# Performance work log

Measured on AMD Instinct MI355X. Metric: run time of the kernel, lower is better.

The kernel has to match this reference:

```python
import jax, jax.numpy as jnp
import numpy as np

HEADS = 8
DIM_HEAD = 64


def setup_inputs() -> dict:
    key = jax.random.key(0)
    ks = jax.random.split(key, 6)
    B, Nq, Nk, Dq = 4, 2048, 2048, 1024
    inner = HEADS * DIM_HEAD  # 512
    return {
        "x": jax.random.normal(ks[0], (B, Nq, Dq), jnp.float32),
        "context": jax.random.normal(ks[1], (B, Nk, Dq), jnp.float32),
        "Wq": jax.random.normal(ks[2], (Dq, inner), jnp.float32) * 0.02,
        "Wkv": jax.random.normal(ks[3], (Dq, 2 * inner), jnp.float32) * 0.02,
        "Wout": jax.random.normal(ks[4], (inner, Dq), jnp.float32) * 0.02,
        "bout": jax.random.normal(ks[5], (Dq,), jnp.float32) * 0.02,
        "topk": 64,
    }


def reference(x, context, Wq, Wkv, Wout, bout, topk):
    B, Nq, _ = x.shape
    Nk = context.shape[1]
    H, D = HEADS, DIM_HEAD
    scale = D ** -0.5

    # projections: b n (h d) -> b h n d
    q = (x @ Wq).reshape(B, Nq, H, D).transpose(0, 2, 1, 3)
    kv = context @ Wkv
    k, v = jnp.split(kv, 2, axis=-1)
    k = k.reshape(B, Nk, H, D).transpose(0, 2, 1, 3)
    v = v.reshape(B, Nk, H, D).transpose(0, 2, 1, 3)

    sim = jnp.einsum('bhid,bhjd->bhij', q, k) * scale  # [B,H,Nq,Nk]

    # top-k sparsification: keep only topk keys per query, mask rest to -max
    k_eff = min(int(topk), Nk)
    _, idx = jax.lax.top_k(sim, k_eff)  # [B,H,Nq,k_eff]
    keep = jnp.zeros(sim.shape, dtype=bool)
    bi = jnp.arange(B)[:, None, None, None]
    hi = jnp.arange(H)[None, :, None, None]
    qi = jnp.arange(Nq)[None, None, :, None]
    keep = keep.at[bi, hi, qi, idx].set(True)
    max_neg = -jnp.finfo(sim.dtype).max
    sim = jnp.where(keep, sim, max_neg)

    attn = jax.nn.softmax(sim, axis=-1)
    out = jnp.einsum('bhij,bhjd->bhid', attn, v)
    out = out.transpose(0, 2, 1, 3).reshape(B, Nq, H * D)
    return out @ Wout + bout
```

## Files before the change

kernel.cpp:

```cpp
#include <hip/hip_runtime.h>
#include <math.h>

#define BATCH 4
#define NQ 2048
#define NK 2048
#define DQ 1024
#define NHEADS 8
#define DHEAD 64
#define INNER (NHEADS*DHEAD)
#define NROWS (BATCH*NHEADS*NQ)
#define CAND_MAX 128

using frag_ab = __attribute__((ext_vector_type(8))) short;
using frag_cd = __attribute__((ext_vector_type(4))) float;
using u16x8   = __attribute__((ext_vector_type(8))) unsigned short;

static __device__ __forceinline__ unsigned short f32_to_bf16_rne(float f) {
  unsigned u = __float_as_uint(f);
  u += 0x7FFFu + ((u >> 16) & 1u);
  return (unsigned short)(u >> 16);
}

static __device__ __forceinline__ void split_trunc(float f, unsigned short& h, unsigned short& l) {
  unsigned u = __float_as_uint(f);
  h = (unsigned short)(u >> 16);
  float hf = __uint_as_float(u & 0xFFFF0000u);
  unsigned r = __float_as_uint(f - hf);
  l = (unsigned short)(r >> 16);
}

static __device__ __forceinline__ void split3(float f, unsigned short& h,
                                              unsigned short& m, unsigned short& l) {
  unsigned u = __float_as_uint(f);
  h = (unsigned short)(u >> 16);
  float hf = __uint_as_float(u & 0xFFFF0000u);
  float r1 = f - hf;
  unsigned u1 = __float_as_uint(r1);
  m = (unsigned short)(u1 >> 16);
  float mf = __uint_as_float(u1 & 0xFFFF0000u);
  float r2 = r1 - mf;
  l = (unsigned short)(__float_as_uint(r2) >> 16);
}

__global__ __launch_bounds__(256) void split_wT3(
    const float* __restrict__ W, int ldw, int coloff, int K, int N,
    unsigned short* __restrict__ TH, unsigned short* __restrict__ TM,
    unsigned short* __restrict__ TL)
{
  __shared__ float tile[32*33];
  const int k0 = blockIdx.x * 32, n0 = blockIdx.y * 32;
  const int t = threadIdx.x;
  {
    int lk = t >> 3, ln4 = (t & 7) * 4;
    const float4 v = *(const float4*)(W + (size_t)(k0 + lk)*ldw + coloff + n0 + ln4);
    tile[lk*33 + ln4+0] = v.x;
    tile[lk*33 + ln4+1] = v.y;
    tile[lk*33 + ln4+2] = v.z;
    tile[lk*33 + ln4+3] = v.w;
  }
  __syncthreads();
  int n = t >> 3, k4 = (t & 7) * 4;
  #pragma unroll
  for (int j = 0; j < 4; ++j) {
    unsigned short h, m, l;
    split3(tile[(k4+j)*33 + n], h, m, l);
    size_t o = (size_t)(n0 + n)*K + k0 + k4 + j;
    TH[o] = h; TM[o] = m; TL[o] = l;
  }
}

__global__ __launch_bounds__(256) void split_wT(
    const float* __restrict__ W, int ldw, int coloff, int K, int N,
    unsigned short* __restrict__ TH, unsigned short* __restrict__ TL)
{
  __shared__ float tile[32*33];
  const int k0 = blockIdx.x * 32, n0 = blockIdx.y * 32;
  const int t = threadIdx.x;
  {
    int lk = t >> 3, ln4 = (t & 7) * 4;
    const float4 v = *(const float4*)(W + (size_t)(k0 + lk)*ldw + coloff + n0 + ln4);
    tile[lk*33 + ln4+0] = v.x;
    tile[lk*33 + ln4+1] = v.y;
    tile[lk*33 + ln4+2] = v.z;
    tile[lk*33 + ln4+3] = v.w;
  }
  __syncthreads();
  int n = t >> 3, k4 = (t & 7) * 4;
  #pragma unroll
  for (int j = 0; j < 4; ++j) {
    unsigned short h, l;
    split_trunc(tile[(k4+j)*33 + n], h, l);
    TH[(size_t)(n0 + n)*K + k0 + k4 + j] = h;
    TL[(size_t)(n0 + n)*K + k0 + k4 + j] = l;
  }
}

__global__ __launch_bounds__(512) void gemm_mfma6_proj(
    const float* __restrict__ A,
    const unsigned short* __restrict__ BtH, const unsigned short* __restrict__ BtM,
    const unsigned short* __restrict__ BtL,
    float* __restrict__ C32,
    unsigned short* __restrict__ Hi, unsigned short* __restrict__ Lo)
{
  extern __shared__ unsigned short smp[];
  unsigned short* ah = smp;
  unsigned short* am = ah + 128*40;
  unsigned short* al = am + 128*40;
  unsigned short* bh = al + 128*40;
  unsigned short* bm = bh + 64*40;
  unsigned short* bl = bm + 64*40;

  const int t = threadIdx.x;
  const int w = t >> 6, l = t & 63;
  const int lr = l & 15, quad = l >> 4;
  const int bid = (int)blockIdx.x;
  const int lid = (bid & 7) * 64 + (bid >> 3);
  const int n0 = (lid & 7) * 64, m0 = (lid >> 3) * 128;

  frag_cd acc[4];
  #pragma unroll
  for (int nt = 0; nt < 4; ++nt)
    acc[nt] = (frag_cd){0.f, 0.f, 0.f, 0.f};

  for (int kt = 0; kt < DQ; kt += 32) {
    {
      int row = t >> 2, k8 = (t & 3) * 8;
      const float* src = A + (size_t)(m0 + row) * DQ + kt + k8;
      float4 v0 = *(const float4*)(src);
      float4 v1 = *(const float4*)(src + 4);
      float vv[8] = {v0.x, v0.y, v0.z, v0.w, v1.x, v1.y, v1.z, v1.w};
      unsigned short h8[8], m8[8], l8[8];
      #pragma unroll
      for (int j = 0; j < 8; ++j) split3(vv[j], h8[j], m8[j], l8[j]);
      *(u16x8*)(ah + row*40 + k8) = *(u16x8*)h8;
      *(u16x8*)(am + row*40 + k8) = *(u16x8*)m8;
      *(u16x8*)(al + row*40 + k8) = *(u16x8*)l8;
    }
    if (t < 256) {
      int n = t >> 2, k8 = (t & 3) * 8;
      size_t o = (size_t)(n0 + n)*DQ + kt + k8;
      *(u16x8*)(bh + n*40 + k8) = *(const u16x8*)(BtH + o);
      *(u16x8*)(bm + n*40 + k8) = *(const u16x8*)(BtM + o);
      *(u16x8*)(bl + n*40 + k8) = *(const u16x8*)(BtL + o);
    }
    __syncthreads();
    {
      int row = w*16 + lr;
      frag_ab aH = *(const frag_ab*)(ah + row*40 + quad*8);
      frag_ab aM = *(const frag_ab*)(am + row*40 + quad*8);
      frag_ab aL = *(const frag_ab*)(al + row*40 + quad*8);
      #pragma unroll
      for (int nt = 0; nt < 4; ++nt) {
        int bn = nt*16 + lr;
        frag_ab bH_ = *(const frag_ab*)(bh + bn*40 + quad*8);
        frag_ab bM_ = *(const frag_ab*)(bm + bn*40 + quad*8);
        frag_ab bL_ = *(const frag_ab*)(bl + bn*40 + quad*8);
        frag_cd c = acc[nt];
        c = __builtin_amdgcn_mfma_f32_16x16x32_bf16(aL, bH_, c, 0, 0, 0);
        c = __builtin_amdgcn_mfma_f32_16x16x32_bf16(aH, bL_, c, 0, 0, 0);
        c = __builtin_amdgcn_mfma_f32_16x16x32_bf16(aM, bM_, c, 0, 0, 0);
        c = __builtin_amdgcn_mfma_f32_16x16x32_bf16(aM, bH_, c, 0, 0, 0);
        c = __builtin_amdgcn_mfma_f32_16x16x32_bf16(aH, bM_, c, 0, 0, 0);
        c = __builtin_amdgcn_mfma_f32_16x16x32_bf16(aH, bH_, c, 0, 0, 0);
        acc[nt] = c;
      }
    }
    __syncthreads();
  }

  #pragma unroll
  for (int nt = 0; nt < 4; ++nt) {
    int cc = n0 + nt*16 + lr;
    int h = cc >> 6, d = cc & 63;
    #pragma unroll
    for (int i = 0; i < 4; ++i) {
      int r = m0 + w*16 + quad*4 + i;
      int b = r >> 11, n = r & (NQ - 1);
      size_t idx = (((size_t)(b*NHEADS + h))*NQ + n)*64 + d;
      float vf = acc[nt][i];
      C32[idx] = vf;
      unsigned short hb = f32_to_bf16_rne(vf);
      float hf = __uint_as_float((unsigned)hb << 16);
      unsigned short lb = f32_to_bf16_rne(vf - hf);
      Hi[idx] = hb;
      Lo[idx] = lb;
    }
  }
}

template<int MODE>
__global__ __launch_bounds__(256) void gemm_mfma3(
    const float* __restrict__ A, int lda,
    const unsigned short* __restrict__ BtH, const unsigned short* __restrict__ BtL,
    int K, int N, const float* __restrict__ bias, float* __restrict__ C0)
{
  __shared__ unsigned short ah[128*72];
  __shared__ unsigned short al[128*72];
  __shared__ unsigned short bh2[64*72];
  __shared__ unsigned short bl2[64*72];
  const int t = threadIdx.x;
  const int w = t >> 6, l = t & 63;
  const int lr = l & 15, quad = l >> 4;
  const int n0 = blockIdx.x * 64, m0 = blockIdx.y * 128;

  frag_cd acc[2][4];
  #pragma unroll
  for (int ms = 0; ms < 2; ++ms)
    #pragma unroll
    for (int nt = 0; nt < 4; ++nt)
      acc[ms][nt] = (frag_cd){0.f, 0.f, 0.f, 0.f};

  for (int kt = 0; kt < K; kt += 64) {
    #pragma unroll
    for (int i = 0; i < 4; ++i) {
      int idx = i*256 + t;
      int row = idx >> 3, k8 = (idx & 7) * 8;
      const float* src = A + (size_t)(m0 + row) * lda + kt + k8;
      float4 v0 = *(const float4*)(src);
      float4 v1 = *(const float4*)(src + 4);
      float vv[8] = {v0.x, v0.y, v0.z, v0.w, v1.x, v1.y, v1.z, v1.w};
      unsigned short h8[8], l8[8];
      #pragma unroll
      for (int j = 0; j < 8; ++j) split_trunc(vv[j], h8[j], l8[j]);
      *(u16x8*)(ah + row*72 + k8) = *(u16x8*)h8;
      *(u16x8*)(al + row*72 + k8) = *(u16x8*)l8;
    }
    #pragma unroll
    for (int i = 0; i < 2; ++i) {
      int idx = i*256 + t;
      int n = idx >> 3, k8 = (idx & 7) * 8;
      *(u16x8*)(bh2 + n*72 + k8) = *(const u16x8*)(BtH + (size_t)(n0 + n)*K + kt + k8);
      *(u16x8*)(bl2 + n*72 + k8) = *(const u16x8*)(BtL + (size_t)(n0 + n)*K + kt + k8);
    }
    __syncthreads();
    #pragma unroll
    for (int ks = 0; ks < 2; ++ks) {
      frag_ab aH[2], aL[2], bH[4], bL[4];
      #pragma unroll
      for (int ms = 0; ms < 2; ++ms) {
        int row = w*32 + ms*16 + lr;
        aH[ms] = *(const frag_ab*)(ah + row*72 + ks*32 + quad*8);
        aL[ms] = *(const frag_ab*)(al + row*72 + ks*32 + quad*8);
      }
      #pragma unroll
      for (int nt = 0; nt < 4; ++nt) {
        int row = nt*16 + lr;
        bH[nt] = *(const frag_ab*)(bh2 + row*72 + ks*32 + quad*8);
        bL[nt] = *(const frag_ab*)(bl2 + row*72 + ks*32 + quad*8);
      }
      #pragma unroll
      for (int ms = 0; ms < 2; ++ms)
        #pragma unroll
        for (int nt = 0; nt < 4; ++nt) {
          acc[ms][nt] = __builtin_amdgcn_mfma_f32_16x16x32_bf16(aH[ms], bH[nt], acc[ms][nt], 0, 0, 0);
          acc[ms][nt] = __builtin_amdgcn_mfma_f32_16x16x32_bf16(aH[ms], bL[nt], acc[ms][nt], 0, 0, 0);
          acc[ms][nt] = __builtin_amdgcn_mfma_f32_16x16x32_bf16(aL[ms], bH[nt], acc[ms][nt], 0, 0, 0);
        }
    }
    __syncthreads();
  }

  #pragma unroll
  for (int ms = 0; ms < 2; ++ms)
    #pragma unroll
    for (int nt = 0; nt < 4; ++nt) {
      int cc = n0 + nt*16 + lr;
      #pragma unroll
      for (int i = 0; i < 4; ++i) {
        int r = m0 + w*32 + ms*16 + quad*4 + i;
        float v = acc[ms][nt][i];
        if (MODE == 0) {
          C0[(size_t)r * N + cc] = v + bias[cc];
        } else {
          int b = r >> 11, n = r & (NQ - 1);
          int h = cc >> 6, d = cc & 63;
          C0[(((size_t)(b*NHEADS + h))*NK + n)*64 + d] = v;
        }
      }
    }
}

__global__ __launch_bounds__(256) void score_mfma(
    const unsigned short* __restrict__ Qhi, const unsigned short* __restrict__ Qlo,
    const unsigned short* __restrict__ Khi, const unsigned short* __restrict__ Klo,
    unsigned short* __restrict__ S16, int bh0)
{
  extern __shared__ unsigned short sm[];
  unsigned short* qh = sm;
  unsigned short* ql = qh + 128*72;
  unsigned short* kh = ql + 128*72;
  unsigned short* kl = kh + 128*72;

  const int t  = threadIdx.x;
  const int qt = blockIdx.x, kt = blockIdx.y;
  const int bh = bh0 + blockIdx.z;
  const size_t qbase = ((size_t)bh*NQ + qt*128) * 64;
  const size_t kbase = ((size_t)bh*NK + kt*128) * 64;

  #pragma unroll
  for (int i = 0; i < 4; ++i) {
    int c   = t + i*256;
    int row = c >> 3, off = (c & 7) * 8;
    *(u16x8*)(qh + row*72 + off) = *(const u16x8*)(Qhi + qbase + row*64 + off);
    *(u16x8*)(ql + row*72 + off) = *(const u16x8*)(Qlo + qbase + row*64 + off);
    *(u16x8*)(kh + row*72 + off) = *(const u16x8*)(Khi + kbase + row*64 + off);
    *(u16x8*)(kl + row*72 + off) = *(const u16x8*)(Klo + kbase + row*64 + off);
  }
  __syncthreads();

  const int w = t >> 6, l = t & 63;
  const int quad = l >> 4, lr = l & 15;

  frag_ab aH[2][2], aL[2][2];
  #pragma unroll
  for (int qs = 0; qs < 2; ++qs) {
    int row = w*32 + qs*16 + lr;
    #pragma unroll
    for (int s = 0; s < 2; ++s) {
      aH[qs][s] = *(const frag_ab*)(qh + row*72 + s*32 + quad*8);
      aL[qs][s] = *(const frag_ab*)(ql + row*72 + s*32 + quad*8);
    }
  }

  for (int ks = 0; ks < 8; ++ks) {
    frag_ab bH[2], bL[2];
    int krow = ks*16 + lr;
    #pragma unroll
    for (int s = 0; s < 2; ++s) {
      bH[s] = *(const frag_ab*)(kh + krow*72 + s*32 + quad*8);
      bL[s] = *(const frag_ab*)(kl + krow*72 + s*32 + quad*8);
    }
    #pragma unroll
    for (int qs = 0; qs < 2; ++qs) {
      frag_cd c = {0.f, 0.f, 0.f, 0.f};
      #pragma unroll
      for (int s = 0; s < 2; ++s) {
        c = __builtin_amdgcn_mfma_f32_16x16x32_bf16(aH[qs][s], bH[s], c, 0, 0, 0);
        c = __builtin_amdgcn_mfma_f32_16x16x32_bf16(aH[qs][s], bL[s], c, 0, 0, 0);
        c = __builtin_amdgcn_mfma_f32_16x16x32_bf16(aL[qs][s], bH[s], c, 0, 0, 0);
      }
      int qrow = qt*128 + w*32 + qs*16 + quad*4;
      int kcol = kt*128 + ks*16 + lr;
      size_t base = ((size_t)blockIdx.z * NQ + qrow) * NK + kcol;
      #pragma unroll
      for (int i = 0; i < 4; ++i) {
        _Float16 h = (_Float16)(c[i] * 0.125f);
        S16[base + (size_t)i*NK] = __builtin_bit_cast(unsigned short, h);
      }
    }
  }
}

__global__ __launch_bounds__(256) void select_rows(
    const unsigned short* __restrict__ S16, unsigned short* __restrict__ cand,
    int* __restrict__ cnt, const int* __restrict__ topkp, int row0)
{
  const int t = threadIdx.x;
  const int w = t >> 6, l = t & 63;
  const int rl = blockIdx.x * 4 + w;
  const size_t row = (size_t)row0 + rl;
  const unsigned short* Sr = S16 + (size_t)rl * NK;
  const unsigned long long lmask = (1ull << l) - 1ull;

  int kEff = *topkp;
  if (kEff > CAND_MAX) kEff = CAND_MAX;
  if (kEff < 1) kEff = 1;

  unsigned uv[32];
  #pragma unroll
  for (int c = 0; c < 32; ++c) {
    unsigned bb = Sr[c*64 + l];
    uv[c] = (bb & 0x8000u) ? (~bb & 0xFFFFu) : (bb | 0x8000u);
  }
  unsigned lo_ = 0u, hi_ = 0xFFFFu;
  while (lo_ < hi_) {
    unsigned mid = (lo_ + hi_ + 1u) >> 1;
    int c_ = 0;
    #pragma unroll
    for (int c = 0; c < 32; ++c) c_ += (uv[c] >= mid) ? 1 : 0;
    #pragma unroll
    for (int off = 32; off > 0; off >>= 1) c_ += __shfl_xor(c_, off);
    if (c_ >= kEff) lo_ = mid; else hi_ = mid - 1;
  }
  unsigned short sb = (lo_ & 0x8000u) ? (unsigned short)(lo_ & 0x7FFFu)
                                      : (unsigned short)(~lo_ & 0xFFFFu);
  float skth = (float)__builtin_bit_cast(_Float16, sb);
  float smarg = skth - 3e-3f;
  _Float16 hm = (_Float16)smarg;
  unsigned short mb = __builtin_bit_cast(unsigned short, hm);
  unsigned um = (mb & 0x8000u) ? (~(unsigned)mb & 0xFFFFu) : ((unsigned)mb | 0x8000u);

  int base = 0;
  for (int c = 0; c < 32; ++c) {
    bool pred = (uv[c] >= um);
    unsigned long long msk = __ballot(pred);
    if (pred) {
      int pos = base + __popcll(msk & lmask);
      if (pos < CAND_MAX) cand[row*CAND_MAX + pos] = (unsigned short)(c*64 + l);
    }
    base += __popcll(msk);
  }
  if (l == 0) cnt[row] = (base < CAND_MAX) ? base : CAND_MAX;
}

__global__ __launch_bounds__(256) void attn_phase_b(
    const float* __restrict__ Q32, const float* __restrict__ K32,
    const float* __restrict__ V32, const unsigned short* __restrict__ cand,
    const int* __restrict__ cnt, float* __restrict__ inner,
    const int* __restrict__ topkp)
{
  __shared__ uint2 pvbuf[4][128];

  const int t = threadIdx.x;
  const int w = t >> 6, l = t & 63;
  const int nwg = (int)gridDim.x;
  const int bid = (int)blockIdx.x;
  const int swz = (bid & 7) * (nwg >> 3) + (bid >> 3);
  const size_t row = (size_t)swz * 4 + w;
  const int bh = (int)(row >> 11);
  const int q  = (int)(row & (NQ - 1));
  const unsigned long long lmask = (1ull << l) - 1ull;

  int kEff = *topkp;
  if (kEff > CAND_MAX) kEff = CAND_MAX;
  if (kEff < 1) kEff = 1;
  int m = cnt[row];
  if (kEff > m) kEff = m;

  const float* Kb = K32 + (size_t)bh * NK * 64;
  const float* Vb = V32 + (size_t)bh * NK * 64;

  const int g = l >> 3, r = l & 7;
  double2 q2[4];
  #pragma unroll
  for (int i = 0; i < 4; ++i) {
    float2 qf = *(const float2*)(Q32 + row*64 + i*16 + r*2);
    q2[i].x = (double)qf.x;
    q2[i].y = (double)qf.y;
  }

  int ck[2];
  ck[0] = cand[row*CAND_MAX + l];
  ck[1] = cand[row*CAND_MAX + 64 + l];
  double cs[2] = {-INFINITY, -INFINITY};
  unsigned long long cu[2] = {0ull, 0ull};

  #define RESCORE_PASS(P, C)                                                  \
  {                                                                           \
    const int j = (P)*8 + g;                                                  \
    const bool valid = (j < m);                                               \
    int key = __shfl(ck[C], j & 63);                                          \
    const float* kp = Kb + (size_t)(valid ? key : 0) * 64;                    \
    double s0 = 0.0, s1 = 0.0;                                                \
    _Pragma("unroll")                                                         \
    for (int i = 0; i < 4; ++i) {                                             \
      float2 kv = *(const float2*)(kp + i*16 + r*2);                          \
      s0 = fma((double)kv.x, q2[i].x, s0);                                    \
      s1 = fma((double)kv.y, q2[i].y, s1);                                    \
    }                                                                         \
    double s = s0 + s1;                                                       \
    s += __shfl_xor(s, 1);                                                    \
    s += __shfl_xor(s, 2);                                                    \
    s += __shfl_xor(s, 4);                                                    \
    s *= 0.125;                                                               \
    double sc = __shfl(s, (l & 7) * 8);                                       \
    const int pp = (P) & 7;                                                   \
    if ((l >> 3) == pp && ((C)*64 + pp*8 + (l & 7)) < m) {                    \
      unsigned long long b = (unsigned long long)__double_as_longlong(sc);    \
      cs[C] = sc;                                                             \
      cu[C] = (b >> 63) ? ~b : (b | 0x8000000000000000ull);                   \
    }                                                                         \
  }

  if (m <= 64) {
    #pragma unroll
    for (int p = 0; p < 8; ++p) RESCORE_PASS(p, 0)
  } else {
    #pragma unroll
    for (int p = 0; p < 8; ++p) RESCORE_PASS(p, 0)
    const int np2 = 8 + ((m - 64 + 7) >> 3);
    for (int p = 8; p < np2; ++p) RESCORE_PASS(p, 1)
  }
  #undef RESCORE_PASS

  const unsigned hu0 = (unsigned)(cu[0] >> 32), lu0 = (unsigned)cu[0];
  const unsigned hu1 = (unsigned)(cu[1] >> 32), lu1 = (unsigned)cu[1];

  unsigned T32 = 0u;
  for (int bit = 31; bit >= 0; --bit) {
    unsigned cT = T32 | (1u << bit);
    int tot = __popcll(__ballot(hu0 >= cT)) + __popcll(__ballot(hu1 >= cT));
    if (tot >= kEff) T32 = cT;
  }
  unsigned Tlo;
  {
    int cgt32 = __popcll(__ballot(hu0 > T32)) + __popcll(__ballot(hu1 > T32));
    bool e0 = (hu0 == T32), e1 = (hu1 == T32);
    unsigned long long bm0 = __ballot(e0), bm1 = __ballot(e1);
    int ceq = __popcll(bm0) + __popcll(bm1);
    int nEq32 = kEff - cgt32;
    if (ceq == 1) {
      Tlo = bm0 ? __shfl(lu0, (int)__builtin_ctzll(bm0))
                : __shfl(lu1, (int)__builtin_ctzll(bm1));
    } else {
      unsigned TL = 0u;
      for (int bit = 31; bit >= 0; --bit) {
        unsigned cT = TL | (1u << bit);
        int tot = __popcll(__ballot(e0 && lu0 >= cT))
                + __popcll(__ballot(e1 && lu1 >= cT));
        if (tot >= nEq32) TL = cT;
      }
      Tlo = TL;
    }
  }
  const unsigned long long T = ((unsigned long long)T32 << 32) | Tlo;

  double s_kth;
  { unsigned long long bb = (T >> 63) ? (T & 0x7FFFFFFFFFFFFFFFull) : ~T;
    s_kth = __longlong_as_double((long long)bb); }

  double nx = -INFINITY;
  #pragma unroll
  for (int c = 0; c < 2; ++c) { double v = (cu[c] < T) ? cs[c] : -INFINITY; nx = fmax(nx, v); }
  #pragma unroll
  for (int off = 32; off > 0; off >>= 1) nx = fmax(nx, __shfl_xor(nx, off));

  double smax = fmax(cs[0], cs[1]);
  #pragma unroll
  for (int off = 32; off > 0; off >>= 1) smax = fmax(smax, __shfl_xor(smax, off));

  const double DELTA = 5e-6;
  float wgt[2];
  if (!(s_kth - nx < 2.0*DELTA)) {
    int cgt = __popcll(__ballot(cu[0] > T)) + __popcll(__ballot(cu[1] > T));
    int nEq = kEff - cgt;
    int eqBase = 0;
    #pragma unroll
    for (int c = 0; c < 2; ++c) {
      bool eq = (cu[c] == T);
      unsigned long long eqm = __ballot(eq);
      int er = __popcll(eqm & lmask);
      bool sel = (cu[c] > T) || (eq && (eqBase + er) < nEq);
      eqBase += __popcll(eqm);
      wgt[c] = sel ? expf((float)(cs[c] - smax)) : 0.f;
    }
  } else {
    double cmid = 0.5 * (s_kth + nx);
    #pragma unroll
    for (int c = 0; c < 2; ++c) {
      double mu = 0.5 + (cs[c] - cmid) / (2.0*DELTA);
      mu = fmin(1.0, fmax(0.0, mu));
      wgt[c] = (float)mu * expf((float)(cs[c] - smax));
    }
  }

  pvbuf[w][l]      = make_uint2((unsigned)ck[0] & (NK - 1), __float_as_uint(wgt[0]));
  pvbuf[w][64 + l] = make_uint2((unsigned)ck[1] & (NK - 1), __float_as_uint(wgt[1]));
  float wsum = wgt[0] + wgt[1];
  #pragma unroll
  for (int off = 32; off > 0; off >>= 1) wsum += __shfl_xor(wsum, off);
  asm volatile("s_waitcnt lgkmcnt(0)" ::: "memory");

  const int sub = l >> 4;
  const int dl  = l & 15;
  const float* Vb4 = Vb + dl * 4;
  float ax = 0.f, ay = 0.f, az = 0.f, aw = 0.f;
  const int mm4 = (m + 3) & ~3;
  #pragma unroll 4
  for (int j0 = 0; j0 < mm4; j0 += 4) {
    uint2 p = pvbuf[w][j0 + sub];
    float wj = __uint_as_float(p.y);
    const float4 v = *(const float4*)(Vb4 + ((size_t)p.x << 6));
    ax = fmaf(wj, v.x, ax);
    ay = fmaf(wj, v.y, ay);
    az = fmaf(wj, v.z, az);
    aw = fmaf(wj, v.w, aw);
  }
  #pragma unroll
  for (int off = 32; off >= 16; off >>= 1) {
    ax += __shfl_xor(ax, off);
    ay += __shfl_xor(ay, off);
    az += __shfl_xor(az, off);
    aw += __shfl_xor(aw, off);
  }
  if (sub == 0) {
    int b = bh >> 3, h = bh & 7;
    float inv = 1.0f / wsum;
    float4 o;
    o.x = ax * inv; o.y = ay * inv; o.z = az * inv; o.w = aw * inv;
    *(float4*)(inner + ((size_t)b*NQ + q)*INNER + h*DHEAD + dl*4) = o;
  }
}

extern "C" void kernel_launch(void* const* d_in, const int* in_sizes, int n_in,
                              void* d_out, int out_size, void* d_ws, size_t ws_size,
                              hipStream_t stream)
{
  const float* x    = (const float*)d_in[0];
  const float* ctx  = (const float*)d_in[1];
  const float* Wq   = (const float*)d_in[2];
  const float* Wkv  = (const float*)d_in[3];
  const float* Wout = (const float*)d_in[4];
  const float* bout = (const float*)d_in[5];
  const int*   topk = (const int*)d_in[6];
  float* out = (float*)d_out;

  const size_t SZ = (size_t)BATCH * NHEADS * NQ * DHEAD;

  size_t off = 0;
  char* base = (char*)d_ws;
  auto take = [&](size_t bytes) { char* r = base + off; off += (bytes + 255) & ~(size_t)255; return r; };
  float* Q32 = (float*)take(SZ * sizeof(float));
  float* K32 = (float*)take(SZ * sizeof(float));
  unsigned short* cand = (unsigned short*)take((size_t)NROWS * CAND_MAX * 2);
  int* cnt = (int*)take((size_t)NROWS * sizeof(int));
  unsigned short* Qhi = (unsigned short*)take(SZ * 2);
  unsigned short* Qlo = (unsigned short*)take(SZ * 2);
  unsigned short* Khi = (unsigned short*)take(SZ * 2);
  unsigned short* Klo = (unsigned short*)take(SZ * 2);
  char* slab = base + off;

  const size_t WSZ = (size_t)INNER * DQ * 2;
  unsigned short* WqTH = (unsigned short*)(slab + 0*WSZ);
  unsigned short* WqTM = (unsigned short*)(slab + 1*WSZ);
  unsigned short* WqTL = (unsigned short*)(slab + 2*WSZ);
  unsigned short* WkTH = (unsigned short*)(slab + 3*WSZ);
  unsigned short* WkTM = (unsigned short*)(slab + 4*WSZ);
  unsigned short* WkTL = (unsigned short*)(slab + 5*WSZ);
  unsigned short* S16 = (unsigned short*)slab;
  unsigned short* WvTH = (unsigned short*)(slab + 0*WSZ);
  unsigned short* WvTL = (unsigned short*)(slab + 1*WSZ);
  unsigned short* WoTH = (unsigned short*)(slab + 2*WSZ);
  unsigned short* WoTL = (unsigned short*)(slab + 3*WSZ);
  float* V32   = (float*)Qhi;
  float* inner = (float*)Khi;

  const size_t per_bh = (size_t)NQ * NK * sizeof(unsigned short);
  size_t avail = (ws_size > off) ? (ws_size - off) : 0;
  int bhchunk = (int)(avail / per_bh);
  if (bhchunk < 1)  bhchunk = 1;
  if (bhchunk > 32) bhchunk = 32;

  const int M = BATCH * NQ;
  const int SCORE_LDS = 4 * 128 * 72 * (int)sizeof(unsigned short);
  const int PROJ_LDS  = 6 * 64 * 40 * (int)sizeof(unsigned short) * 2;
  hipFuncSetAttribute(reinterpret_cast<const void*>(score_mfma),
                      hipFuncAttributeMaxDynamicSharedMemorySize, SCORE_LDS);
  hipFuncSetAttribute(reinterpret_cast<const void*>(gemm_mfma6_proj),
                      hipFuncAttributeMaxDynamicSharedMemorySize, PROJ_LDS);

  split_wT3<<<dim3(DQ/32, INNER/32), 256, 0, stream>>>(Wq,  INNER,   0, DQ, INNER, WqTH, WqTM, WqTL);
  split_wT3<<<dim3(DQ/32, INNER/32), 256, 0, stream>>>(Wkv, 2*INNER, 0, DQ, INNER, WkTH, WkTM, WkTL);

  gemm_mfma6_proj<<<dim3((INNER/64)*(M/128)), 512, PROJ_LDS, stream>>>(x,   WqTH, WqTM, WqTL, Q32, Qhi, Qlo);
  gemm_mfma6_proj<<<dim3((INNER/64)*(M/128)), 512, PROJ_LDS, stream>>>(ctx, WkTH, WkTM, WkTL, K32, Khi, Klo);

  for (int c0 = 0; c0 < BATCH*NHEADS; c0 += bhchunk) {
    int cc = BATCH*NHEADS - c0; if (cc > bhchunk) cc = bhchunk;
    score_mfma<<<dim3(NQ/128, NK/128, cc), 256, SCORE_LDS, stream>>>(
        Qhi, Qlo, Khi, Klo, S16, c0);
    select_rows<<<dim3(cc*NQ/4), 256, 0, stream>>>(S16, cand, cnt, topk, c0*NQ);
  }

  split_wT<<<dim3(DQ/32, INNER/32), 256, 0, stream>>>(Wkv, 2*INNER, INNER, DQ, INNER, WvTH, WvTL);
  split_wT<<<dim3(INNER/32, DQ/32), 256, 0, stream>>>(Wout, DQ, 0, INNER, DQ, WoTH, WoTL);

  gemm_mfma3<2><<<dim3(INNER/64, M/128), 256, 0, stream>>>(ctx, DQ, WvTH, WvTL, DQ, INNER, nullptr, V32);
  attn_phase_b<<<dim3(NROWS/4), 256, 0, stream>>>(Q32, K32, V32, cand, cnt, inner, topk);
  gemm_mfma3<0><<<dim3(DQ/64, M/128), 256, 0, stream>>>(inner, INNER, WoTH, WoTL, INNER, DQ, bout, out);
}
```

Measured before the change: 723.0 us.

## Store score tiles in permuted layout with 16-byte vector writes and reads

The QK score kernel now keeps all eight k-slice accumulators per row in registers and writes each row's values as one 16-byte vector instead of scattered 2-byte stores. This produces a permuted column layout within each 128-key tile. The select kernel reads its 32 values per lane as four 16-byte loads and maps each candidate position back to the true key index through a bit permutation. This trades more accumulator registers for coalesced wide memory traffic on the large fp16 score buffer.

```diff
diff --git a/kernel.cpp b/kernel.cpp
--- a/kernel.cpp
+++ b/kernel.cpp
@@ -322,6 +322,8 @@
     }
   }
 
+  frag_cd c[2][8];
+  #pragma unroll
   for (int ks = 0; ks < 8; ++ks) {
     frag_ab bH[2], bL[2];
     int krow = ks*16 + lr;
@@ -332,23 +334,31 @@
     }
     #pragma unroll
     for (int qs = 0; qs < 2; ++qs) {
-      frag_cd c = {0.f, 0.f, 0.f, 0.f};
+      frag_cd cc = {0.f, 0.f, 0.f, 0.f};
       #pragma unroll
       for (int s = 0; s < 2; ++s) {
-        c = __builtin_amdgcn_mfma_f32_16x16x32_bf16(aH[qs][s], bH[s], c, 0, 0, 0);
-        c = __builtin_amdgcn_mfma_f32_16x16x32_bf16(aH[qs][s], bL[s], c, 0, 0, 0);
-        c = __builtin_amdgcn_mfma_f32_16x16x32_bf16(aL[qs][s], bH[s], c, 0, 0, 0);
-      }
-      int qrow = qt*128 + w*32 + qs*16 + quad*4;
-      int kcol = kt*128 + ks*16 + lr;
-      size_t base = ((size_t)blockIdx.z * NQ + qrow) * NK + kcol;
-      #pragma unroll
-      for (int i = 0; i < 4; ++i) {
-        _Float16 h = (_Float16)(c[i] * 0.125f);
-        S16[base + (size_t)i*NK] = __builtin_bit_cast(unsigned short, h);
-      }
-    }
-  }
+        cc = __builtin_amdgcn_mfma_f32_16x16x32_bf16(aH[qs][s], bH[s], cc, 0, 0, 0);
+        cc = __builtin_amdgcn_mfma_f32_16x16x32_bf16(aH[qs][s], bL[s], cc, 0, 0, 0);
+        cc = __builtin_amdgcn_mfma_f32_16x16x32_bf16(aL[qs][s], bH[s], cc, 0, 0, 0);
+      }
+      c[qs][ks] = cc;
+    }
+  }
+
+  #pragma unroll
+  for (int qs = 0; qs < 2; ++qs)
+    #pragma unroll
+    for (int i = 0; i < 4; ++i) {
+      unsigned short o8[8];
+      #pragma unroll
+      for (int ks = 0; ks < 8; ++ks) {
+        _Float16 h = (_Float16)(c[qs][ks][i] * 0.125f);
+        o8[ks] = __builtin_bit_cast(unsigned short, h);
+      }
+      int qrow = qt*128 + w*32 + qs*16 + quad*4 + i;
+      size_t base = ((size_t)blockIdx.z * NQ + qrow) * NK + kt*128 + lr*8;
+      *(u16x8*)(S16 + base) = *(u16x8*)o8;
+    }
 }
 
 __global__ __launch_bounds__(256) void select_rows(
@@ -366,10 +376,15 @@
   if (kEff > CAND_MAX) kEff = CAND_MAX;
   if (kEff < 1) kEff = 1;
 
+  u16x8 ch[4];
+  #pragma unroll
+  for (int k = 0; k < 4; ++k)
+    ch[k] = *(const u16x8*)(Sr + (size_t)l*32 + k*8);
+
   unsigned uv[32];
   #pragma unroll
   for (int c = 0; c < 32; ++c) {
-    unsigned bb = Sr[c*64 + l];
+    unsigned bb = (unsigned)(unsigned short)ch[c >> 3][c & 7];
     uv[c] = (bb & 0x8000u) ? (~bb & 0xFFFFu) : (bb | 0x8000u);
   }
   unsigned lo_ = 0u, hi_ = 0xFFFFu;
@@ -396,7 +411,11 @@
     unsigned long long msk = __ballot(pred);
     if (pred) {
       int pos = base + __popcll(msk & lmask);
-      if (pos < CAND_MAX) cand[row*CAND_MAX + pos] = (unsigned short)(c*64 + l);
+      if (pos < CAND_MAX) {
+        unsigned p = (unsigned)l * 32u + (unsigned)c;
+        unsigned key = (p & 0xFF80u) | ((p & 7u) << 4) | ((p >> 3) & 15u);
+        cand[row*CAND_MAX + pos] = (unsigned short)key;
+      }
     }
     base += __popcll(msk);
   }
```

After: 899.8 us. +24.5%, slower.

## Restructure split-bf16 GEMM to 512 threads, K-step 32, and XCD-aware block swizzle

Applied to the files above, without the earlier changes.

The V-projection and output GEMMs now launch 512-thread blocks, with each wave computing a 16x64 slice instead of 32x64. The K loop steps by 32 instead of 64, which shrinks LDS tiles to a 40-element row pitch. A 1D grid with a bid&7 remap groups neighbouring tiles onto the same XCD to improve L2 reuse. More waves per block should hide latency better, but the smaller K step doubles the number of barriers and halves MFMA work per synchronisation.

```diff
diff --git a/kernel.cpp b/kernel.cpp
--- a/kernel.cpp
+++ b/kernel.cpp
@@ -189,32 +189,32 @@
 }
 
 template<int MODE>
-__global__ __launch_bounds__(256) void gemm_mfma3(
+__global__ __launch_bounds__(512) void gemm_mfma3(
     const float* __restrict__ A, int lda,
     const unsigned short* __restrict__ BtH, const unsigned short* __restrict__ BtL,
     int K, int N, const float* __restrict__ bias, float* __restrict__ C0)
 {
-  __shared__ unsigned short ah[128*72];
-  __shared__ unsigned short al[128*72];
-  __shared__ unsigned short bh2[64*72];
-  __shared__ unsigned short bl2[64*72];
+  __shared__ unsigned short ah[128*40];
+  __shared__ unsigned short al[128*40];
+  __shared__ unsigned short bh2[64*40];
+  __shared__ unsigned short bl2[64*40];
   const int t = threadIdx.x;
   const int w = t >> 6, l = t & 63;
   const int lr = l & 15, quad = l >> 4;
-  const int n0 = blockIdx.x * 64, m0 = blockIdx.y * 128;
-
-  frag_cd acc[2][4];
-  #pragma unroll
-  for (int ms = 0; ms < 2; ++ms)
-    #pragma unroll
-    for (int nt = 0; nt < 4; ++nt)
-      acc[ms][nt] = (frag_cd){0.f, 0.f, 0.f, 0.f};
-
-  for (int kt = 0; kt < K; kt += 64) {
-    #pragma unroll
-    for (int i = 0; i < 4; ++i) {
-      int idx = i*256 + t;
-      int row = idx >> 3, k8 = (idx & 7) * 8;
+  const int nx = N >> 6;
+  const int bid = (int)blockIdx.x;
+  const int nwg = (int)gridDim.x;
+  const int lid = (bid & 7) * (nwg >> 3) + (bid >> 3);
+  const int n0 = (lid % nx) * 64, m0 = (lid / nx) * 128;
+
+  frag_cd acc[4];
+  #pragma unroll
+  for (int nt = 0; nt < 4; ++nt)
+    acc[nt] = (frag_cd){0.f, 0.f, 0.f, 0.f};
+
+  for (int kt = 0; kt < K; kt += 32) {
+    {
+      int row = t >> 2, k8 = (t & 3) * 8;
       const float* src = A + (size_t)(m0 + row) * lda + kt + k8;
       float4 v0 = *(const float4*)(src);
       float4 v1 = *(const float4*)(src + 4);
@@ -222,62 +222,49 @@
       unsigned short h8[8], l8[8];
       #pragma unroll
       for (int j = 0; j < 8; ++j) split_trunc(vv[j], h8[j], l8[j]);
-      *(u16x8*)(ah + row*72 + k8) = *(u16x8*)h8;
-      *(u16x8*)(al + row*72 + k8) = *(u16x8*)l8;
-    }
-    #pragma unroll
-    for (int i = 0; i < 2; ++i) {
-      int idx = i*256 + t;
-      int n = idx >> 3, k8 = (idx & 7) * 8;
-      *(u16x8*)(bh2 + n*72 + k8) = *(const u16x8*)(BtH + (size_t)(n0 + n)*K + kt + k8);
-      *(u16x8*)(bl2 + n*72 + k8) = *(const u16x8*)(BtL + (size_t)(n0 + n)*K + kt + k8);
+      *(u16x8*)(ah + row*40 + k8) = *(u16x8*)h8;
+      *(u16x8*)(al + row*40 + k8) = *(u16x8*)l8;
+    }
+    if (t < 256) {
+      int n = t >> 2, k8 = (t & 3) * 8;
+      size_t o = (size_t)(n0 + n)*K + kt + k8;
+      *(u16x8*)(bh2 + n*40 + k8) = *(const u16x8*)(BtH + o);
+      *(u16x8*)(bl2 + n*40 + k8) = *(const u16x8*)(BtL + o);
     }
     __syncthreads();
-    #pragma unroll
-    for (int ks = 0; ks < 2; ++ks) {
-      frag_ab aH[2], aL[2], bH[4], bL[4];
-      #pragma unroll
-      for (int ms = 0; ms < 2; ++ms) {
-        int row = w*32 + ms*16 + lr;
-        aH[ms] = *(const frag_ab*)(ah + row*72 + ks*32 + quad*8);
-        aL[ms] = *(const frag_ab*)(al + row*72 + ks*32 + quad*8);
-      }
+    {
+      int row = w*16 + lr;
+      frag_ab aH = *(const frag_ab*)(ah + row*40 + quad*8);
+      frag_ab aL = *(const frag_ab*)(al + row*40 + quad*8);
       #pragma unroll
       for (int nt = 0; nt < 4; ++nt) {
-        int row = nt*16 + lr;
-        bH[nt] = *(const frag_ab*)(bh2 + row*72 + ks*32 + quad*8);
-        bL[nt] = *(const frag_ab*)(bl2 + row*72 + ks*32 + quad*8);
+        int bn = nt*16 + lr;
+        frag_ab bH_ = *(const frag_ab*)(bh2 + bn*40 + quad*8);
+        frag_ab bL_ = *(const frag_ab*)(bl2 + bn*40 + quad*8);
+        acc[nt] = __builtin_amdgcn_mfma_f32_16x16x32_bf16(aH, bH_, acc[nt], 0, 0, 0);
+        acc[nt] = __builtin_amdgcn_mfma_f32_16x16x32_bf16(aH, bL_, acc[nt], 0, 0, 0);
+        acc[nt] = __builtin_amdgcn_mfma_f32_16x16x32_bf16(aL, bH_, acc[nt], 0, 0, 0);
       }
-      #pragma unroll
-      for (int ms = 0; ms < 2; ++ms)
-        #pragma unroll
-        for (int nt = 0; nt < 4; ++nt) {
-          acc[ms][nt] = __builtin_amdgcn_mfma_f32_16x16x32_bf16(aH[ms], bH[nt], acc[ms][nt], 0, 0, 0);
-          acc[ms][nt] = __builtin_amdgcn_mfma_f32_16x16x32_bf16(aH[ms], bL[nt], acc[ms][nt], 0, 0, 0);
-          acc[ms][nt] = __builtin_amdgcn_mfma_f32_16x16x32_bf16(aL[ms], bH[nt], acc[ms][nt], 0, 0, 0);
-        }
     }
     __syncthreads();
   }
 
   #pragma unroll
-  for (int ms = 0; ms < 2; ++ms)
-    #pragma unroll
-    for (int nt = 0; nt < 4; ++nt) {
-      int cc = n0 + nt*16 + lr;
-      #pragma unroll
-      for (int i = 0; i < 4; ++i) {
-        int r = m0 + w*32 + ms*16 + quad*4 + i;
-        float v = acc[ms][nt][i];
-        if (MODE == 0) {
-          C0[(size_t)r * N + cc] = v + bias[cc];
-        } else {
-          int b = r >> 11, n = r & (NQ - 1);
-          int h = cc >> 6, d = cc & 63;
-          C0[(((size_t)(b*NHEADS + h))*NK + n)*64 + d] = v;
-        }
+  for (int nt = 0; nt < 4; ++nt) {
+    int cc = n0 + nt*16 + lr;
+    #pragma unroll
+    for (int i = 0; i < 4; ++i) {
+      int r = m0 + w*16 + quad*4 + i;
+      float v = acc[nt][i];
+      if (MODE == 0) {
+        C0[(size_t)r * N + cc] = v + bias[cc];
+      } else {
+        int b = r >> 11, n = r & (NQ - 1);
+        int h = cc >> 6, d = cc & 63;
+        C0[(((size_t)(b*NHEADS + h))*NK + n)*64 + d] = v;
       }
     }
+  }
 }
 
 __global__ __launch_bounds__(256) void score_mfma(
@@ -665,7 +652,7 @@
   split_wT<<<dim3(DQ/32, INNER/32), 256, 0, stream>>>(Wkv, 2*INNER, INNER, DQ, INNER, WvTH, WvTL);
   split_wT<<<dim3(INNER/32, DQ/32), 256, 0, stream>>>(Wout, DQ, 0, INNER, DQ, WoTH, WoTL);
 
-  gemm_mfma3<2><<<dim3(INNER/64, M/128), 256, 0, stream>>>(ctx, DQ, WvTH, WvTL, DQ, INNER, nullptr, V32);
+  gemm_mfma3<2><<<dim3((INNER/64)*(M/128)), 512, 0, stream>>>(ctx, DQ, WvTH, WvTL, DQ, INNER, nullptr, V32);
   attn_phase_b<<<dim3(NROWS/4), 256, 0, stream>>>(Q32, K32, V32, cand, cnt, inner, topk);
-  gemm_mfma3<0><<<dim3(DQ/64, M/128), 256, 0, stream>>>(inner, INNER, WoTH, WoTL, INNER, DQ, bout, out);
-}
+  gemm_mfma3<0><<<dim3((DQ/64)*(M/128)), 512, 0, stream>>>(inner, INNER, WoTH, WoTL, INNER, DQ, bout, out);
+}
```

After: 719.8 us. About the same (-0.4%).
